# Optimization experiments

Hardware: AMD Instinct MI355X
Metric: run time of the kernel (lower is better)

## Reference

```python
import jax, jax.numpy as jnp
import numpy as np

T, E, F, H, B = 3, 500000, 128, 64, 1024

def setup_inputs() -> dict:
    key = jax.random.key(0)
    k1, k2, k3, k4 = jax.random.split(key, 4)
    edge_attr = jax.random.normal(k1, (T, E, F), dtype=jnp.float32)
    batch = jax.random.randint(k2, (T, E), 0, B, dtype=jnp.int32)
    W1 = jax.random.normal(k3, (T, F, H), dtype=jnp.float32) * 0.08
    b1 = jnp.zeros((T, H), dtype=jnp.float32)
    W2 = jax.random.normal(k4, (T, H), dtype=jnp.float32) * 0.1
    b2 = jnp.zeros((T,), dtype=jnp.float32)
    return {"edge_attr": edge_attr, "batch": batch, "W1": W1, "b1": b1,
            "W2": W2, "b2": b2, "num_graphs": B}

def reference(edge_attr, batch, W1, b1, W2, b2, num_graphs):
    # Per edge type: MLP score -> per-graph segment softmax -> weighted scatter-sum.
    # Dropout is identity at eval time.
    def pool_one(ea, be, w1, bb1, w2, bb2):
        h = jnp.tanh(ea @ w1 + bb1)                 # [E, H]
        score = h @ w2 + bb2                        # [E]
        smax = jax.ops.segment_max(score, be, num_segments=num_graphs)  # [B]
        ex = jnp.exp(score - smax[be])              # stable softmax numerator
        ssum = jax.ops.segment_sum(ex, be, num_segments=num_graphs)    # [B]
        attn = ex / ssum[be]                        # [E]
        msgs = attn[:, None] * ea                   # [E, F]
        return jax.ops.segment_sum(msgs, be, num_segments=num_graphs)  # [B, F]
    pooled = jax.vmap(pool_one)(edge_attr, batch, W1, b1, W2, b2)      # [T, B, F]
    return pooled.mean(axis=0)                      # [B, F]
```

## Files before the change

kernel.cpp:

```cpp
#include <hip/hip_runtime.h>

#define T 3
#define E 500000
#define F 128
#define H 64
#define B 1024

#define BLK_E 64
#define EMASK 0x7FFFF
#define PB 1024

typedef __attribute__((ext_vector_type(4))) float f32x4;
typedef __fp16 h2 __attribute__((ext_vector_type(2)));
typedef __fp16 h8 __attribute__((ext_vector_type(8)));
union H4 {
  h2 p[2];
  uint2 d;
};
union HS {
  __fp16 h;
  unsigned short s;
};


__device__ __forceinline__ float tanh_fast(float x) {
  float e = __expf(2.0f * x);
  return 1.0f - 2.0f / (e + 1.0f);
}
__device__ __forceinline__ void bar_lds() {
  asm volatile("s_waitcnt lgkmcnt(0)" ::: "memory");
  __builtin_amdgcn_s_barrier();
  __builtin_amdgcn_sched_barrier(0);
}


__global__ void k_init(const float* __restrict__ W1, float* __restrict__ acc,
                       float* __restrict__ ssum, unsigned* __restrict__ cnt,
                       unsigned short* __restrict__ Wpack) {
  int idx = blockIdx.x * blockDim.x + threadIdx.x;
  if (idx < T * B * F) acc[idx] = 0.0f;
  if (idx < T * B) {
    ssum[idx] = 0.0f;
    cnt[idx] = 0u;
  }
  if (idx < T * 4 * 4 * 64) {
    int lane = idx & 63;
    int r2 = idx >> 6;
    int ks = r2 & 3;
    int nt = (r2 >> 2) & 3;
    int t = r2 >> 4;
    int j = nt * 16 + (lane & 15);
#pragma unroll
    for (int e = 0; e < 8; ++e) {
      int f = ks * 32 + (lane >> 4) * 8 + e;
      HS hs;
      hs.h = (__fp16)W1[((size_t)t * F + f) * H + j];
      Wpack[(size_t)idx * 8 + e] = hs.s;
    }
  }
}


__global__ __launch_bounds__(256) void k_hist(
    const int* __restrict__ batch, unsigned* __restrict__ cnt) {
  __shared__ unsigned h[B];
  int t = blockIdx.y;
  for (int i = threadIdx.x; i < B; i += 256) h[i] = 0u;
  __syncthreads();
  int base = blockIdx.x * 16384;
  int end = base + 16384 < E ? base + 16384 : E;
  for (int i = base + threadIdx.x; i < end; i += 256)
    atomicAdd(&h[batch[(size_t)t * E + i]], 1u);
  __syncthreads();
  for (int i = threadIdx.x; i < B; i += 256) {
    unsigned v = h[i];
    if (v) atomicAdd(&cnt[t * B + i], v);
  }
}


__global__ void k_scan(const unsigned* __restrict__ cnt,
                       unsigned* __restrict__ cursor) {
  __shared__ unsigned wsum[16];
  int tid = threadIdx.x;
  int t = blockIdx.x;
  unsigned v = cnt[t * B + tid];
  unsigned x = v;
#pragma unroll
  for (int d = 1; d < 64; d <<= 1) {
    unsigned y = __shfl_up(x, d);
    if ((tid & 63) >= d) x += y;
  }
  if ((tid & 63) == 63) wsum[tid >> 6] = x;
  __syncthreads();
  if (tid < 16) {
    unsigned s = wsum[tid];
#pragma unroll
    for (int d = 1; d < 16; d <<= 1) {
      unsigned y = __shfl_up(s, d);
      if (tid >= d) s += y;
    }
    wsum[tid] = s;
  }
  __syncthreads();
  unsigned base = (tid >> 6) ? wsum[(tid >> 6) - 1] : 0u;
  cursor[t * B + tid] = base + x - v;
}


__global__ __launch_bounds__(256) void k_scatter(
    const int* __restrict__ batch, unsigned* __restrict__ cursor,
    unsigned* __restrict__ eid) {
  __shared__ unsigned hloc[B];
  __shared__ unsigned baseg[B];
  int t = blockIdx.y;
  int base = blockIdx.x * 1024;
  for (int i = threadIdx.x; i < B; i += 256) hloc[i] = 0u;
  __syncthreads();
  int bb[4];
  unsigned rk[4];
#pragma unroll
  for (int k = 0; k < 4; ++k) {
    int e = base + k * 256 + threadIdx.x;
    if (e < E) {
      bb[k] = batch[(size_t)t * E + e];
      rk[k] = atomicAdd(&hloc[bb[k]], 1u);
    }
  }
  __syncthreads();
  for (int i = threadIdx.x; i < B; i += 256) {
    unsigned cv = hloc[i];
    if (cv) baseg[i] = atomicAdd(&cursor[t * B + i], cv);
  }
  __syncthreads();
#pragma unroll
  for (int k = 0; k < 4; ++k) {
    int e = base + k * 256 + threadIdx.x;
    if (e < E)
      eid[(size_t)t * E + baseg[bb[k]] + rk[k]] =
          (unsigned)e | ((unsigned)bb[k] << 19);
  }
}


__global__ __launch_bounds__(256, 3) void k_fused(
    const float* __restrict__ ea, const unsigned* __restrict__ eid,
    const unsigned short* __restrict__ Wpack, const float* __restrict__ b1,
    const float* __restrict__ W2, const float* __restrict__ b2,
    float* __restrict__ accg, float* __restrict__ ssum) {
  __shared__ unsigned short xh_t[BLK_E * F];
  __shared__ unsigned short xl_t[BLK_E * F];
  __shared__ float scl[BLK_E];
  __shared__ int eidl[3][BLK_E];
  __shared__ int bblb[3][BLK_E];

  int t = blockIdx.y;
  int tid = threadIdx.x;
  const int NT = (E + BLK_E - 1) / BLK_E;
  const int CH = (NT + PB - 1) / PB;
  int t0 = blockIdx.x * CH;
  int n = NT - t0;
  if (n <= 0) return;
  if (n > CH) n = CH;

  const float* eag = ea + (size_t)t * E * (size_t)F;
  const unsigned* eidt = eid + (size_t)t * E;
  int l = tid & 63;
  int w = tid >> 6;
  int c = tid & 31;
  int r0 = tid >> 5;
  int jb = l & 15;

  const unsigned short* wpt = Wpack + (size_t)t * 8192;
  h8 bh[4][4];
#pragma unroll
  for (int nt = 0; nt < 4; ++nt)
#pragma unroll
    for (int ks = 0; ks < 4; ++ks)
      bh[nt][ks] = *(const h8*)(wpt + ((nt * 4 + ks) * 64 + l) * 8);
  float b1r[4], w2r[4];
#pragma unroll
  for (int nt = 0; nt < 4; ++nt) {
    b1r[nt] = b1[t * H + nt * 16 + jb];
    w2r[nt] = W2[t * H + nt * 16 + jb];
  }
  float b2t = b2[t];

  if (tid < BLK_E) {
    int p0 = t0 * BLK_E + tid;
    if (p0 >= E) p0 = E - 1;
    unsigned pk = eidt[p0];
    eidl[0][tid] = (int)(pk & EMASK);
    bblb[0][tid] = (int)(pk >> 19);
    int p1 = (t0 + 1) * BLK_E + tid;
    if (p1 >= E) p1 = E - 1;
    pk = eidt[p1];
    eidl[1][tid] = (int)(pk & EMASK);
    bblb[1][tid] = (int)(pk >> 19);
  }
  __syncthreads();

  float4 v[8];
#pragma unroll
  for (int k = 0; k < 8; ++k) {
    int id = eidl[0][k * 8 + r0];
    v[k] = *(const float4*)(eag + (size_t)id * F + 4 * c);
  }

  int wv = tid >> 6;
  int ll = tid & 63;
  float* acct = accg + (size_t)t * B * F;
  float a0 = 0.f, a1 = 0.f, asum = 0.f;
  int prev = -1;

  for (int i = 0; i < n; ++i) {
    int ib = i % 3;
    int e0 = (t0 + i) * BLK_E;

#pragma unroll
    for (int k = 0; k < 8; ++k) {
      int r = k * 8 + r0;
      float4 x = v[k];
      H4 hv, lv;
      hv.p[0] = __builtin_amdgcn_cvt_pkrtz(x.x, x.y);
      hv.p[1] = __builtin_amdgcn_cvt_pkrtz(x.z, x.w);
      lv.p[0] = __builtin_amdgcn_cvt_pkrtz(x.x - (float)hv.p[0][0],
                                           x.y - (float)hv.p[0][1]);
      lv.p[1] = __builtin_amdgcn_cvt_pkrtz(x.z - (float)hv.p[1][0],
                                           x.w - (float)hv.p[1][1]);
      int off = (r * 256 + c * 8) ^ ((r & 7) << 4);
      *(uint2*)((char*)xh_t + off) = hv.d;
      *(uint2*)((char*)xl_t + off) = lv.d;
    }
    bar_lds();

    unsigned pk_next = 0;
    if (tid < BLK_E) {
      int p = (t0 + i + 2) * BLK_E + tid;
      if (p >= E) p = E - 1;
      pk_next = eidt[p];
    }
    if (i + 1 < n) {
      int nb = (i + 1) % 3;
#pragma unroll
      for (int k = 0; k < 8; ++k) {
        int id = eidl[nb][k * 8 + r0];
        v[k] = *(const float4*)(eag + (size_t)id * F + 4 * c);
      }
    }

    f32x4 acc[4];
#pragma unroll
    for (int nt = 0; nt < 4; ++nt) acc[nt] = (f32x4){0.f, 0.f, 0.f, 0.f};
    int arow = w * 16 + (l & 15);
    int abase = arow * 256;
    int aswz = (arow & 7) << 4;
#pragma unroll
    for (int ks = 0; ks < 4; ++ks) {
      int abyte = (abase + (ks * 32 + (l >> 4) * 8) * 2) ^ aswz;
      h8 ah = *(const h8*)((const char*)xh_t + abyte);
      h8 al = *(const h8*)((const char*)xl_t + abyte);
#pragma unroll
      for (int nt = 0; nt < 4; ++nt) {
        acc[nt] = __builtin_amdgcn_mfma_f32_16x16x32_f16(ah, bh[nt][ks],
                                                         acc[nt], 0, 0, 0);
        acc[nt] = __builtin_amdgcn_mfma_f32_16x16x32_f16(al, bh[nt][ks],
                                                         acc[nt], 0, 0, 0);
      }
    }

    float p0 = 0.f, p1 = 0.f, p2 = 0.f, p3 = 0.f;
#pragma unroll
    for (int nt = 0; nt < 4; ++nt) {
      p0 = fmaf(tanh_fast(acc[nt][0] + b1r[nt]), w2r[nt], p0);
      p1 = fmaf(tanh_fast(acc[nt][1] + b1r[nt]), w2r[nt], p1);
      p2 = fmaf(tanh_fast(acc[nt][2] + b1r[nt]), w2r[nt], p2);
      p3 = fmaf(tanh_fast(acc[nt][3] + b1r[nt]), w2r[nt], p3);
    }
#pragma unroll
    for (int m = 1; m < 16; m <<= 1) {
      p0 += __shfl_xor(p0, m);
      p1 += __shfl_xor(p1, m);
      p2 += __shfl_xor(p2, m);
      p3 += __shfl_xor(p3, m);
    }
    if (jb == 0) {
      int rb = w * 16 + (l >> 4) * 4;
      *(float4*)&scl[rb] = (float4){p0, p1, p2, p3};
    }
    bar_lds();

    for (int ii = 0; ii < 16; ++ii) {
      int eloc = wv * 16 + ii;
      if (e0 + eloc >= E) break;
      int b = bblb[ib][eloc];
      if (b != prev) {
        if (prev >= 0) {
          atomicAdd(acct + (size_t)prev * F + 2 * ll, a0);
          atomicAdd(acct + (size_t)prev * F + 2 * ll + 1, a1);
          if (ll == 0) atomicAdd(&ssum[t * B + prev], asum);
        }
        prev = b;
        a0 = 0.f;
        a1 = 0.f;
        asum = 0.f;
      }
      float exv = __expf(scl[eloc] + b2t);
      int off = (eloc * 256 + ll * 4) ^ ((eloc & 7) << 4);
      h2 xh = *(const h2*)((const char*)xh_t + off);
      h2 xl = *(const h2*)((const char*)xl_t + off);
      float x0 = (float)xh[0] + (float)xl[0];
      float x1 = (float)xh[1] + (float)xl[1];
      a0 = fmaf(x0, exv, a0);
      a1 = fmaf(x1, exv, a1);
      asum += exv;
    }

    if (tid < BLK_E) {
      eidl[(i + 2) % 3][tid] = (int)(pk_next & EMASK);
      bblb[(i + 2) % 3][tid] = (int)(pk_next >> 19);
    }
    bar_lds();
  }

  if (prev >= 0) {
    atomicAdd(acct + (size_t)prev * F + 2 * ll, a0);
    atomicAdd(acct + (size_t)prev * F + 2 * ll + 1, a1);
    if (ll == 0) atomicAdd(&ssum[t * B + prev], asum);
  }
}


__global__ __launch_bounds__(256) void k_final(
    const float* __restrict__ acc, const float* __restrict__ ssum,
    float* __restrict__ out) {
  int idx = blockIdx.x * 256 + threadIdx.x;
  if (idx >= B * F) return;
  int b = idx >> 7;
  float s = 0.0f;
#pragma unroll
  for (int t = 0; t < T; ++t)
    s += acc[(size_t)t * B * F + idx] / ssum[t * B + b];
  out[idx] = s * (1.0f / 3.0f);
}


extern "C" void kernel_launch(void* const* d_in, const int* in_sizes, int n_in,
                              void* d_out, int out_size, void* d_ws, size_t ws_size,
                              hipStream_t stream) {
  const float* ea    = (const float*)d_in[0];
  const int*   batch = (const int*)d_in[1];
  const float* W1    = (const float*)d_in[2];
  const float* b1    = (const float*)d_in[3];
  const float* W2    = (const float*)d_in[4];
  const float* b2    = (const float*)d_in[5];
  float* out = (float*)d_out;

  float*          acc    = (float*)d_ws;
  float*          ssum   = acc + (size_t)T * B * F;
  unsigned*       cnt    = (unsigned*)(ssum + T * B);
  unsigned*       cursor = cnt + T * B;
  unsigned*       eid    = cursor + T * B;
  unsigned short* Wpack  = (unsigned short*)(eid + (size_t)T * E);

  k_init<<<(T * B * F + 255) / 256, 256, 0, stream>>>(W1, acc, ssum, cnt, Wpack);

  dim3 gh((E + 16383) / 16384, T);
  k_hist<<<gh, 256, 0, stream>>>(batch, cnt);
  k_scan<<<T, B, 0, stream>>>(cnt, cursor);
  dim3 ge((E + 1023) / 1024, T);
  k_scatter<<<ge, 256, 0, stream>>>(batch, cursor, eid);

  dim3 gs(PB, T);
  k_fused<<<gs, 256, 0, stream>>>(ea, eid, Wpack, b1, W2, b2, acc, ssum);

  k_final<<<(B * F + 255) / 256, 256, 0, stream>>>(acc, ssum, out);
}
```

Baseline: 288.2 us.

## Double edge tile to 128 and split hidden dim across 512-thread blocks

```diff
diff --git a/kernel.cpp b/kernel.cpp
--- a/kernel.cpp
+++ b/kernel.cpp
@@ -6,9 +6,9 @@
 #define H 64
 #define B 1024
 
-#define BLK_E 64
+#define BLK_E 128
 #define EMASK 0x7FFFF
-#define PB 1024
+#define PBX 512
 
 typedef __attribute__((ext_vector_type(4))) float f32x4;
 typedef __fp16 h2 __attribute__((ext_vector_type(2)));
@@ -143,21 +143,21 @@
 }
 
 
-__global__ __launch_bounds__(256, 3) void k_fused(
+__global__ __launch_bounds__(512, 4) void k_fused(
     const float* __restrict__ ea, const unsigned* __restrict__ eid,
     const unsigned short* __restrict__ Wpack, const float* __restrict__ b1,
     const float* __restrict__ W2, const float* __restrict__ b2,
     float* __restrict__ accg, float* __restrict__ ssum) {
   __shared__ unsigned short xh_t[BLK_E * F];
   __shared__ unsigned short xl_t[BLK_E * F];
-  __shared__ float scl[BLK_E];
+  __shared__ float scl2[2][BLK_E];
   __shared__ int eidl[3][BLK_E];
   __shared__ int bblb[3][BLK_E];
 
   int t = blockIdx.y;
   int tid = threadIdx.x;
   const int NT = (E + BLK_E - 1) / BLK_E;
-  const int CH = (NT + PB - 1) / PB;
+  const int CH = (NT + PBX - 1) / PBX;
   int t0 = blockIdx.x * CH;
   int n = NT - t0;
   if (n <= 0) return;
@@ -167,22 +167,24 @@
   const unsigned* eidt = eid + (size_t)t * E;
   int l = tid & 63;
   int w = tid >> 6;
+  int rw = w & 3;
+  int jh = w >> 2;
   int c = tid & 31;
   int r0 = tid >> 5;
   int jb = l & 15;
 
   const unsigned short* wpt = Wpack + (size_t)t * 8192;
-  h8 bh[4][4];
-#pragma unroll
-  for (int nt = 0; nt < 4; ++nt)
+  h8 bh[2][4];
+#pragma unroll
+  for (int n2 = 0; n2 < 2; ++n2)
 #pragma unroll
     for (int ks = 0; ks < 4; ++ks)
-      bh[nt][ks] = *(const h8*)(wpt + ((nt * 4 + ks) * 64 + l) * 8);
-  float b1r[4], w2r[4];
-#pragma unroll
-  for (int nt = 0; nt < 4; ++nt) {
-    b1r[nt] = b1[t * H + nt * 16 + jb];
-    w2r[nt] = W2[t * H + nt * 16 + jb];
+      bh[n2][ks] = *(const h8*)(wpt + (((jh * 2 + n2) * 4 + ks) * 64 + l) * 8);
+  float b1r[2], w2r[2];
+#pragma unroll
+  for (int n2 = 0; n2 < 2; ++n2) {
+    b1r[n2] = b1[t * H + (jh * 2 + n2) * 16 + jb];
+    w2r[n2] = W2[t * H + (jh * 2 + n2) * 16 + jb];
   }
   float b2t = b2[t];
 
@@ -203,7 +205,7 @@
   float4 v[8];
 #pragma unroll
   for (int k = 0; k < 8; ++k) {
-    int id = eidl[0][k * 8 + r0];
+    int id = eidl[0][k * 16 + r0];
     v[k] = *(const float4*)(eag + (size_t)id * F + 4 * c);
   }
 
@@ -219,7 +221,7 @@
 
 #pragma unroll
     for (int k = 0; k < 8; ++k) {
-      int r = k * 8 + r0;
+      int r = k * 16 + r0;
       float4 x = v[k];
       H4 hv, lv;
       hv.p[0] = __builtin_amdgcn_cvt_pkrtz(x.x, x.y);
@@ -244,49 +246,56 @@
       int nb = (i + 1) % 3;
 #pragma unroll
       for (int k = 0; k < 8; ++k) {
-        int id = eidl[nb][k * 8 + r0];
+        int id = eidl[nb][k * 16 + r0];
         v[k] = *(const float4*)(eag + (size_t)id * F + 4 * c);
       }
     }
 
-    f32x4 acc[4];
-#pragma unroll
-    for (int nt = 0; nt < 4; ++nt) acc[nt] = (f32x4){0.f, 0.f, 0.f, 0.f};
-    int arow = w * 16 + (l & 15);
-    int abase = arow * 256;
-    int aswz = (arow & 7) << 4;
+    f32x4 acc[2][2];
+#pragma unroll
+    for (int s = 0; s < 2; ++s)
+#pragma unroll
+      for (int n2 = 0; n2 < 2; ++n2) acc[s][n2] = (f32x4){0.f, 0.f, 0.f, 0.f};
 #pragma unroll
     for (int ks = 0; ks < 4; ++ks) {
-      int abyte = (abase + (ks * 32 + (l >> 4) * 8) * 2) ^ aswz;
-      h8 ah = *(const h8*)((const char*)xh_t + abyte);
-      h8 al = *(const h8*)((const char*)xl_t + abyte);
-#pragma unroll
-      for (int nt = 0; nt < 4; ++nt) {
-        acc[nt] = __builtin_amdgcn_mfma_f32_16x16x32_f16(ah, bh[nt][ks],
-                                                         acc[nt], 0, 0, 0);
-        acc[nt] = __builtin_amdgcn_mfma_f32_16x16x32_f16(al, bh[nt][ks],
-                                                         acc[nt], 0, 0, 0);
-      }
-    }
-
-    float p0 = 0.f, p1 = 0.f, p2 = 0.f, p3 = 0.f;
-#pragma unroll
-    for (int nt = 0; nt < 4; ++nt) {
-      p0 = fmaf(tanh_fast(acc[nt][0] + b1r[nt]), w2r[nt], p0);
-      p1 = fmaf(tanh_fast(acc[nt][1] + b1r[nt]), w2r[nt], p1);
-      p2 = fmaf(tanh_fast(acc[nt][2] + b1r[nt]), w2r[nt], p2);
-      p3 = fmaf(tanh_fast(acc[nt][3] + b1r[nt]), w2r[nt], p3);
-    }
-#pragma unroll
-    for (int m = 1; m < 16; m <<= 1) {
-      p0 += __shfl_xor(p0, m);
-      p1 += __shfl_xor(p1, m);
-      p2 += __shfl_xor(p2, m);
-      p3 += __shfl_xor(p3, m);
-    }
-    if (jb == 0) {
-      int rb = w * 16 + (l >> 4) * 4;
-      *(float4*)&scl[rb] = (float4){p0, p1, p2, p3};
+      int kb = (ks * 32 + (l >> 4) * 8) * 2;
+#pragma unroll
+      for (int s = 0; s < 2; ++s) {
+        int arow = rw * 32 + s * 16 + (l & 15);
+        int abyte = (arow * 256 + kb) ^ ((arow & 7) << 4);
+        h8 ah = *(const h8*)((const char*)xh_t + abyte);
+        h8 al = *(const h8*)((const char*)xl_t + abyte);
+#pragma unroll
+        for (int n2 = 0; n2 < 2; ++n2) {
+          acc[s][n2] = __builtin_amdgcn_mfma_f32_16x16x32_f16(
+              ah, bh[n2][ks], acc[s][n2], 0, 0, 0);
+          acc[s][n2] = __builtin_amdgcn_mfma_f32_16x16x32_f16(
+              al, bh[n2][ks], acc[s][n2], 0, 0, 0);
+        }
+      }
+    }
+
+#pragma unroll
+    for (int s = 0; s < 2; ++s) {
+      float p0 = 0.f, p1 = 0.f, p2 = 0.f, p3 = 0.f;
+#pragma unroll
+      for (int n2 = 0; n2 < 2; ++n2) {
+        p0 = fmaf(tanh_fast(acc[s][n2][0] + b1r[n2]), w2r[n2], p0);
+        p1 = fmaf(tanh_fast(acc[s][n2][1] + b1r[n2]), w2r[n2], p1);
+        p2 = fmaf(tanh_fast(acc[s][n2][2] + b1r[n2]), w2r[n2], p2);
+        p3 = fmaf(tanh_fast(acc[s][n2][3] + b1r[n2]), w2r[n2], p3);
+      }
+#pragma unroll
+      for (int m = 1; m < 16; m <<= 1) {
+        p0 += __shfl_xor(p0, m);
+        p1 += __shfl_xor(p1, m);
+        p2 += __shfl_xor(p2, m);
+        p3 += __shfl_xor(p3, m);
+      }
+      if (jb == 0) {
+        int rb = rw * 32 + s * 16 + (l >> 4) * 4;
+        *(float4*)&scl2[jh][rb] = (float4){p0, p1, p2, p3};
+      }
     }
     bar_lds();
 
@@ -305,7 +314,7 @@
         a1 = 0.f;
         asum = 0.f;
       }
-      float exv = __expf(scl[eloc] + b2t);
+      float exv = __expf(scl2[0][eloc] + scl2[1][eloc] + b2t);
       int off = (eloc * 256 + ll * 4) ^ ((eloc & 7) << 4);
       h2 xh = *(const h2*)((const char*)xh_t + off);
       h2 xl = *(const h2*)((const char*)xl_t + off);
@@ -371,8 +380,8 @@
   dim3 ge((E + 1023) / 1024, T);
   k_scatter<<<ge, 256, 0, stream>>>(batch, cursor, eid);
 
-  dim3 gs(PB, T);
-  k_fused<<<gs, 256, 0, stream>>>(ea, eid, Wpack, b1, W2, b2, acc, ssum);
+  dim3 gs(PBX, T);
+  k_fused<<<gs, 512, 0, stream>>>(ea, eid, Wpack, b1, W2, b2, acc, ssum);
 
   k_final<<<(B * F + 255) / 256, 256, 0, stream>>>(acc, ssum, out);
 }
```

Result: slower. 309.3 us (+7.3%).
